# Kernel tuning notes

Hardware: AMD Instinct MI355X
Metric: run time of the kernel (lower is better)

## Reference

```python
import jax, jax.numpy as jnp
import numpy as np

K = 3          # kernel_size
BOARD = 15     # gomoku board H = W
HOUT = BOARD - K + 1   # 13 windows per spatial dim
DIM_IN = 2 * K * K     # 18 binary features per window -> perfect hash


def fake_quant(x, scale, bits=8):
    """Straight-through fake quantization: round to int grid, clamp to bit range."""
    qmax = 2 ** (bits - 1) - 1
    y = jnp.clip(jnp.round(x * scale), -qmax - 1, qmax) / scale
    return x + jax.lax.stop_gradient(y - x)


def setup_inputs() -> dict:
    key = jax.random.key(0)
    ks = jax.random.split(key, 8)
    B = 8192
    board = jax.random.randint(ks[0], (B, 2, BOARD, BOARD), 0, 2, dtype=jnp.int32)
    emb = jax.random.normal(ks[1], (2 ** 18, 32), dtype=jnp.float32) * 0.05
    w1 = jax.random.normal(ks[2], (32, 32), dtype=jnp.float32) * 0.1
    b1 = jax.random.normal(ks[3], (32,), dtype=jnp.float32) * 0.05
    w2 = jax.random.normal(ks[4], (32, 32), dtype=jnp.float32) * 0.1
    b2 = jax.random.normal(ks[5], (32,), dtype=jnp.float32) * 0.05
    w3 = jax.random.normal(ks[6], (3, 32), dtype=jnp.float32) * 0.1
    b3 = jax.random.normal(ks[7], (3,), dtype=jnp.float32) * 0.05
    return {"board": board, "emb": emb, "w1": w1, "b1": b1,
            "w2": w2, "b2": b2, "w3": w3, "b3": b3}


def reference(board, emb, w1, b1, w2, b2, w3, b3):
    B = board.shape[0]
    # im2col unfold in torch F.unfold order (channel-major, then kernel row, col)
    # patches: (B, HOUT, HOUT, C*K*K)
    patches = jnp.stack(
        [board[:, c, i:i + HOUT, j:j + HOUT]
         for c in range(2) for i in range(K) for j in range(K)], axis=-1)
    # perfect hash of 18 binary features -> index into 2^18 embedding table
    powers = (2 ** jnp.arange(DIM_IN)).astype(jnp.int32)
    idx = jnp.sum(patches * powers, axis=-1)          # (B, HOUT, HOUT)
    feats = emb[idx]                                  # (B, HOUT, HOUT, 32) gather
    feats = fake_quant(jnp.clip(feats, -1.0, 127 / 128), 128.0, bits=8)
    v = jnp.sum(feats, axis=(1, 2))                   # (B, 32) clamp-sum accumulate
    # tiny quantized 3-layer value MLP
    for i, (wt, bs) in enumerate(((w1, b1), (w2, b2), (w3, b3))):
        v = jnp.clip(v, -1.0 if i == 0 else 0.0, 127 / 128)
        wq = fake_quant(wt, 128.0, bits=8)
        bq = fake_quant(bs, 128.0 * 128.0, bits=32)
        v = v @ wq.T + bq
    policy = jnp.zeros((B, BOARD, BOARD), dtype=v.dtype)
    return (v, policy)
```

## Files before the change

### kernel.cpp

```cpp
#include <hip/hip_runtime.h>
#include <stdint.h>

#define NW 169

__device__ __forceinline__ float qw128(float x) {
    float r = rintf(x * 128.f);
    r = fminf(fmaxf(r, -128.f), 127.f);
    return r * 0.0078125f;
}
__device__ __forceinline__ float qb16384(float x) {
    return rintf(x * 16384.f) * 6.103515625e-05f;
}

__global__ void prep_kernel(const float* __restrict__ emb, uint8_t* __restrict__ q,
                            float4* __restrict__ policy) {
    int bid = blockIdx.x;
    int tid = threadIdx.x;
    if (bid >= 2048) {
        int i = (bid - 2048) * 256 + tid;
        policy[i] = make_float4(0.f, 0.f, 0.f, 0.f);
        return;
    }
    int i = bid * 256 + tid;
    const float4* in4 = (const float4*)emb + (size_t)i * 4;
    uint32_t words[4];
#pragma unroll
    for (int t = 0; t < 4; ++t) {
        float4 f = in4[t];
        float v[4] = {f.x, f.y, f.z, f.w};
        uint32_t w = 0;
#pragma unroll
        for (int j = 0; j < 4; ++j) {
            float x = fminf(fmaxf(v[j], -1.f), 0.9921875f);
            int r = (int)rintf(x * 128.f) + 128;
            w |= ((uint32_t)r & 0xFFu) << (8 * j);
        }
        words[t] = w;
    }
    ((uint4*)q)[i] = make_uint4(words[0], words[1], words[2], words[3]);
}

__global__ __launch_bounds__(512, 1)
void nnue_kernel(const int* __restrict__ board,
                 const uint8_t* __restrict__ embq,
                 const float* __restrict__ w1, const float* __restrict__ b1,
                 const float* __restrict__ w2, const float* __restrict__ b2,
                 const float* __restrict__ w3, const float* __restrict__ b3,
                 float* __restrict__ vout)
{
    __shared__ float w1T[32][32], w2T[32][32], w3T[32][4];
    __shared__ float b1q[32], b2q[32], b3q[4];
    __shared__ unsigned long long ballots[8][8];
    __shared__ int hashoff[8][176];
    __shared__ float vlds[8][32], h1lds[8][32], h2lds[8][32];

    int tid = threadIdx.x;
    for (int i = tid; i < 1024; i += 512) {
        int j = i & 31, k = i >> 5;
        w1T[k][j] = qw128(w1[j * 32 + k]);
        w2T[k][j] = qw128(w2[j * 32 + k]);
    }
    if (tid < 96) { int k = tid & 31, j = tid >> 5; w3T[k][j] = qw128(w3[j * 32 + k]); }
    if (tid < 32) { b1q[tid] = qb16384(b1[tid]); b2q[tid] = qb16384(b2[tid]); }
    if (tid < 3)  b3q[tid] = qb16384(b3[tid]);
    __syncthreads();

    int wv = tid >> 6, lane = tid & 63;
    int b = blockIdx.x * 8 + wv;
    const int* bp = board + b * 450;

#pragma unroll
    for (int t = 0; t < 8; ++t) {
        int n = t * 64 + lane;
        int cell = (n < 450) ? bp[n] : 0;
        unsigned long long m = __ballot(cell != 0);
        if (lane == 0) ballots[wv][t] = m;
    }

#pragma unroll
    for (int t = 0; t < 3; ++t) {
        int w = t * 64 + lane;
        if (w < NW) {
            int wi = w / 13;
            int wj = w - wi * 13;
            int idx = 0;
#pragma unroll
            for (int c = 0; c < 2; ++c) {
#pragma unroll
                for (int i = 0; i < 3; ++i) {
                    int s = c * 225 + (wi + i) * 15;
                    int word = s >> 6, off = s & 63;
                    unsigned long long lo = ballots[wv][word];
                    unsigned long long hi = ballots[wv][word + 1];
                    unsigned long long bits = (lo >> off) | ((hi << 1) << (63 - off));
                    idx |= (int)((bits >> wj) & 7ull) << (9 * c + 3 * i);
                }
            }
            hashoff[wv][w] = idx << 5;
        }
    }

    int d2 = lane & 3;
    int g = lane >> 2;
    const uint8_t* base = embq + d2 * 8;
    uint32_t a02lo = 0, a13lo = 0, a02hi = 0, a13hi = 0;
#pragma unroll
    for (int it = 0; it < 11; ++it) {
        int w = it * 16 + g;
        if (w < NW) {
            int off = hashoff[wv][w];
            uint2 dw = *(const uint2*)(base + off);
            a02lo += dw.x & 0x00FF00FFu;
            a13lo += (dw.x >> 8) & 0x00FF00FFu;
            a02hi += dw.y & 0x00FF00FFu;
            a13hi += (dw.y >> 8) & 0x00FF00FFu;
        }
    }
#pragma unroll
    for (int off = 4; off <= 32; off <<= 1) {
        a02lo += __shfl_xor(a02lo, off);
        a13lo += __shfl_xor(a13lo, off);
        a02hi += __shfl_xor(a02hi, off);
        a13hi += __shfl_xor(a13hi, off);
    }
    if (lane < 4) {
        int c[8];
        c[0] = (int)(a02lo & 0xFFFFu) - 21632;
        c[2] = (int)(a02lo >> 16)     - 21632;
        c[1] = (int)(a13lo & 0xFFFFu) - 21632;
        c[3] = (int)(a13lo >> 16)     - 21632;
        c[4] = (int)(a02hi & 0xFFFFu) - 21632;
        c[6] = (int)(a02hi >> 16)     - 21632;
        c[5] = (int)(a13hi & 0xFFFFu) - 21632;
        c[7] = (int)(a13hi >> 16)     - 21632;
#pragma unroll
        for (int j = 0; j < 8; ++j) {
            int cc = min(max(c[j], -128), 127);
            vlds[wv][lane * 8 + j] = (float)cc * 0.0078125f;
        }
    }

    int jj = lane & 31, hf = lane >> 5;
    float s1 = 0.f;
#pragma unroll
    for (int k2 = 0; k2 < 16; ++k2) {
        int k = hf * 16 + k2;
        s1 = fmaf(vlds[wv][k], w1T[k][jj], s1);
    }
    s1 += __shfl_xor(s1, 32);
    s1 += b1q[jj];
    s1 = fminf(fmaxf(s1, 0.f), 0.9921875f);
    if (lane < 32) h1lds[wv][jj] = s1;

    float s2 = 0.f;
#pragma unroll
    for (int k2 = 0; k2 < 16; ++k2) {
        int k = hf * 16 + k2;
        s2 = fmaf(h1lds[wv][k], w2T[k][jj], s2);
    }
    s2 += __shfl_xor(s2, 32);
    s2 += b2q[jj];
    s2 = fminf(fmaxf(s2, 0.f), 0.9921875f);
    if (lane < 32) h2lds[wv][jj] = s2;

    float s3 = 0.f;
    if (jj < 3) {
#pragma unroll
        for (int k2 = 0; k2 < 16; ++k2) {
            int k = hf * 16 + k2;
            s3 = fmaf(h2lds[wv][k], w3T[k][jj], s3);
        }
    }
    s3 += __shfl_xor(s3, 32);
    if (lane < 3) vout[b * 3 + lane] = s3 + b3q[lane];
}

extern "C" void kernel_launch(void* const* d_in, const int* in_sizes, int n_in,
                              void* d_out, int out_size, void* d_ws, size_t ws_size,
                              hipStream_t stream) {
    const int*   board = (const int*)d_in[0];
    const float* emb   = (const float*)d_in[1];
    const float* w1    = (const float*)d_in[2];
    const float* b1    = (const float*)d_in[3];
    const float* w2    = (const float*)d_in[4];
    const float* b2    = (const float*)d_in[5];
    const float* w3    = (const float*)d_in[6];
    const float* b3    = (const float*)d_in[7];
    float* out = (float*)d_out;
    uint8_t* embq = (uint8_t*)d_ws;

    prep_kernel<<<3848, 256, 0, stream>>>(emb, embq, (float4*)(out + 24576));
    nnue_kernel<<<1024, 512, 0, stream>>>(board, embq, w1, b1, w2, b2, w3, b3, out);
}
```

Measured before the change: 37.10 us.

## Widen embedding gathers to 16B, shrink blocks, use nontemporal policy stores

Each lane now gathers a 16-byte half of the 32-byte quantized embedding row instead of 8 bytes. Loads are issued unconditionally into registers, with a clamped window index and a masked tail, so more requests are in flight and branches are avoided. Blocks shrink from 8 to 4 waves with relaxed launch bounds, which doubles the grid and raises occupancy. The policy zero-fill uses nontemporal stores. Accumulators double and the shuffle reduction gains a stage, adding register pressure and extra shuffles.

```diff
diff --git a/kernel.cpp b/kernel.cpp
--- a/kernel.cpp
+++ b/kernel.cpp
@@ -2,6 +2,8 @@
 #include <stdint.h>
 
 #define NW 169
+
+typedef float f32x4 __attribute__((ext_vector_type(4)));
 
 __device__ __forceinline__ float qw128(float x) {
     float r = rintf(x * 128.f);
@@ -13,12 +15,13 @@
 }
 
 __global__ void prep_kernel(const float* __restrict__ emb, uint8_t* __restrict__ q,
-                            float4* __restrict__ policy) {
+                            f32x4* __restrict__ policy) {
     int bid = blockIdx.x;
     int tid = threadIdx.x;
     if (bid >= 2048) {
         int i = (bid - 2048) * 256 + tid;
-        policy[i] = make_float4(0.f, 0.f, 0.f, 0.f);
+        f32x4 z = {0.f, 0.f, 0.f, 0.f};
+        __builtin_nontemporal_store(z, &policy[i]);
         return;
     }
     int i = bid * 256 + tid;
@@ -40,7 +43,7 @@
     ((uint4*)q)[i] = make_uint4(words[0], words[1], words[2], words[3]);
 }
 
-__global__ __launch_bounds__(512, 1)
+__global__ __launch_bounds__(256)
 void nnue_kernel(const int* __restrict__ board,
                  const uint8_t* __restrict__ embq,
                  const float* __restrict__ w1, const float* __restrict__ b1,
@@ -50,12 +53,12 @@
 {
     __shared__ float w1T[32][32], w2T[32][32], w3T[32][4];
     __shared__ float b1q[32], b2q[32], b3q[4];
-    __shared__ unsigned long long ballots[8][8];
-    __shared__ int hashoff[8][176];
-    __shared__ float vlds[8][32], h1lds[8][32], h2lds[8][32];
+    __shared__ unsigned long long ballots[4][8];
+    __shared__ int hashoff[4][192];
+    __shared__ float vlds[4][32], h1lds[4][32], h2lds[4][32];
 
     int tid = threadIdx.x;
-    for (int i = tid; i < 1024; i += 512) {
+    for (int i = tid; i < 1024; i += 256) {
         int j = i & 31, k = i >> 5;
         w1T[k][j] = qw128(w1[j * 32 + k]);
         w2T[k][j] = qw128(w2[j * 32 + k]);
@@ -66,7 +69,7 @@
     __syncthreads();
 
     int wv = tid >> 6, lane = tid & 63;
-    int b = blockIdx.x * 8 + wv;
+    int b = blockIdx.x * 4 + wv;
     const int* bp = board + b * 450;
 
 #pragma unroll
@@ -80,63 +83,70 @@
 #pragma unroll
     for (int t = 0; t < 3; ++t) {
         int w = t * 64 + lane;
-        if (w < NW) {
-            int wi = w / 13;
-            int wj = w - wi * 13;
-            int idx = 0;
-#pragma unroll
-            for (int c = 0; c < 2; ++c) {
-#pragma unroll
-                for (int i = 0; i < 3; ++i) {
-                    int s = c * 225 + (wi + i) * 15;
-                    int word = s >> 6, off = s & 63;
-                    unsigned long long lo = ballots[wv][word];
-                    unsigned long long hi = ballots[wv][word + 1];
-                    unsigned long long bits = (lo >> off) | ((hi << 1) << (63 - off));
-                    idx |= (int)((bits >> wj) & 7ull) << (9 * c + 3 * i);
-                }
+        int wi = w / 13;
+        int wj = w - wi * 13;
+        int idx = 0;
+#pragma unroll
+        for (int c = 0; c < 2; ++c) {
+#pragma unroll
+            for (int i = 0; i < 3; ++i) {
+                int s = c * 225 + (min(wi, 12) + i) * 15;
+                int word = s >> 6, off = s & 63;
+                unsigned long long lo = ballots[wv][word];
+                unsigned long long hi = ballots[wv][word + 1];
+                unsigned long long bits = (lo >> off) | ((hi << 1) << (63 - off));
+                idx |= (int)((bits >> wj) & 7ull) << (9 * c + 3 * i);
             }
-            hashoff[wv][w] = idx << 5;
-        }
-    }
-
-    int d2 = lane & 3;
-    int g = lane >> 2;
-    const uint8_t* base = embq + d2 * 8;
-    uint32_t a02lo = 0, a13lo = 0, a02hi = 0, a13hi = 0;
-#pragma unroll
-    for (int it = 0; it < 11; ++it) {
-        int w = it * 16 + g;
-        if (w < NW) {
-            int off = hashoff[wv][w];
-            uint2 dw = *(const uint2*)(base + off);
-            a02lo += dw.x & 0x00FF00FFu;
-            a13lo += (dw.x >> 8) & 0x00FF00FFu;
-            a02hi += dw.y & 0x00FF00FFu;
-            a13hi += (dw.y >> 8) & 0x00FF00FFu;
-        }
-    }
-#pragma unroll
-    for (int off = 4; off <= 32; off <<= 1) {
-        a02lo += __shfl_xor(a02lo, off);
-        a13lo += __shfl_xor(a13lo, off);
-        a02hi += __shfl_xor(a02hi, off);
-        a13hi += __shfl_xor(a13hi, off);
-    }
-    if (lane < 4) {
-        int c[8];
-        c[0] = (int)(a02lo & 0xFFFFu) - 21632;
-        c[2] = (int)(a02lo >> 16)     - 21632;
-        c[1] = (int)(a13lo & 0xFFFFu) - 21632;
-        c[3] = (int)(a13lo >> 16)     - 21632;
-        c[4] = (int)(a02hi & 0xFFFFu) - 21632;
-        c[6] = (int)(a02hi >> 16)     - 21632;
-        c[5] = (int)(a13hi & 0xFFFFu) - 21632;
-        c[7] = (int)(a13hi >> 16)     - 21632;
-#pragma unroll
-        for (int j = 0; j < 8; ++j) {
-            int cc = min(max(c[j], -128), 127);
-            vlds[wv][lane * 8 + j] = (float)cc * 0.0078125f;
+        }
+        hashoff[wv][w] = (w < NW) ? (idx << 5) : 0;
+    }
+
+    int d1 = lane & 1;
+    int g = lane >> 1;
+    const uint8_t* base = embq + d1 * 16;
+    uint4 dv[6];
+#pragma unroll
+    for (int it = 0; it < 6; ++it) {
+        int w = it * 32 + g;
+        dv[it] = *(const uint4*)(base + hashoff[wv][w]);
+    }
+    const uint32_t M = 0x00FF00FFu;
+    uint32_t a0lo = 0, a0hi = 0, a1lo = 0, a1hi = 0;
+    uint32_t a2lo = 0, a2hi = 0, a3lo = 0, a3hi = 0;
+#pragma unroll
+    for (int it = 0; it < 6; ++it) {
+        uint32_t x0 = dv[it].x, x1 = dv[it].y, x2 = dv[it].z, x3 = dv[it].w;
+        if (it == 5) {
+            uint32_t keep = (160 + g < NW) ? 0xFFFFFFFFu : 0u;
+            x0 &= keep; x1 &= keep; x2 &= keep; x3 &= keep;
+        }
+        a0lo += x0 & M; a0hi += (x0 >> 8) & M;
+        a1lo += x1 & M; a1hi += (x1 >> 8) & M;
+        a2lo += x2 & M; a2hi += (x2 >> 8) & M;
+        a3lo += x3 & M; a3hi += (x3 >> 8) & M;
+    }
+#pragma unroll
+    for (int off = 2; off <= 32; off <<= 1) {
+        a0lo += __shfl_xor(a0lo, off); a0hi += __shfl_xor(a0hi, off);
+        a1lo += __shfl_xor(a1lo, off); a1hi += __shfl_xor(a1hi, off);
+        a2lo += __shfl_xor(a2lo, off); a2hi += __shfl_xor(a2hi, off);
+        a3lo += __shfl_xor(a3lo, off); a3hi += __shfl_xor(a3hi, off);
+    }
+    if (lane < 2) {
+        uint32_t lo[4] = {a0lo, a1lo, a2lo, a3lo};
+        uint32_t hi[4] = {a0hi, a1hi, a2hi, a3hi};
+#pragma unroll
+        for (int j = 0; j < 4; ++j) {
+            int c[4];
+            c[0] = (int)(lo[j] & 0xFFFFu) - 21632;
+            c[1] = (int)(hi[j] & 0xFFFFu) - 21632;
+            c[2] = (int)(lo[j] >> 16)     - 21632;
+            c[3] = (int)(hi[j] >> 16)     - 21632;
+#pragma unroll
+            for (int u = 0; u < 4; ++u) {
+                int cc = min(max(c[u], -128), 127);
+                vlds[wv][d1 * 16 + j * 4 + u] = (float)cc * 0.0078125f;
+            }
         }
     }
 
@@ -189,6 +199,6 @@
     float* out = (float*)d_out;
     uint8_t* embq = (uint8_t*)d_ws;
 
-    prep_kernel<<<3848, 256, 0, stream>>>(emb, embq, (float4*)(out + 24576));
-    nnue_kernel<<<1024, 512, 0, stream>>>(board, embq, w1, b1, w2, b2, w3, b3, out);
-}
+    prep_kernel<<<3848, 256, 0, stream>>>(emb, embq, (f32x4*)(out + 24576));
+    nnue_kernel<<<2048, 256, 0, stream>>>(board, embq, w1, b1, w2, b2, w3, b3, out);
+}
```

New measurement: 40.54 us. +9.3%, slower.
